# Kernel tuning notes

Measured on AMD Instinct MI355X. Metric: run time of the kernel, lower is better.

## Reference

```python
import jax, jax.numpy as jnp
import numpy as np

S, B, H = 512, 256, 500


def setup_inputs() -> dict:
    key = jax.random.key(0)
    k1, k2, k3, k4, k5 = jax.random.split(key, 5)
    return {
        "hidden": jax.random.normal(k1, (1, B, H), dtype=jnp.float32),
        "encoder_output": jax.random.normal(k2, (S, B, H), dtype=jnp.float32),
        "W_attn": jax.random.normal(k3, (H, 2 * H), dtype=jnp.float32) * 0.02,
        "b_attn": jax.random.normal(k4, (H,), dtype=jnp.float32) * 0.02,
        "v": jax.random.normal(k5, (H,), dtype=jnp.float32),
    }


def reference(hidden, encoder_output, W_attn, b_attn, v):
    # hidden: [1, B, H] -> broadcast to [S, B, H]; concat -> [S, B, 2H]
    s, b, h = encoder_output.shape
    h_exp = jnp.broadcast_to(hidden, (s, b, h))
    cat = jnp.concatenate([h_exp, encoder_output], axis=2)  # [S, B, 2H]
    # Linear(2H -> H) with torch convention W: [out, in], then tanh
    energy = jnp.tanh(jnp.einsum("sbi,hi->sbh", cat, W_attn) + b_attn)  # [S, B, H]
    scores = jnp.einsum("sbh,h->sb", energy, v)  # [S, B]
    attn = jax.nn.softmax(scores.T, axis=1)  # [B, S]
    return attn[:, None, :]  # [B, 1, S]
```

## Files before the change

kernel.cpp:

```cpp
#include <hip/hip_runtime.h>
#include <hip/hip_fp16.h>

#define S_DIM 512
#define B_DIM 256
#define H_DIM 500
#define HP    512
#define M_DIM (S_DIM * B_DIM)

typedef _Float16 half8_t __attribute__((ext_vector_type(8)));
typedef float    f32x4  __attribute__((ext_vector_type(4)));

#define WS_W2I 0
#define WS_AT  (512 * 1024)
#define WS_VP  (1024 * 1024)
#define WS_SC  (1024 * 1024 + 4096)

__device__ __forceinline__ void gld_lds16(const void* g, void* l) {
    __builtin_amdgcn_global_load_lds(
        (const __attribute__((address_space(1))) unsigned int*)g,
        (__attribute__((address_space(3))) unsigned int*)l, 16, 0, 0);
}

__global__ void prep_w2_v(const float* __restrict__ W, const float* __restrict__ v,
                          _Float16* __restrict__ W2img, float* __restrict__ vp) {
    int idx = blockIdx.x * blockDim.x + threadIdx.x;
#pragma unroll
    for (int r = 0; r < 2; ++r) {
        int e = idx + r * 131072;
        int n = e >> 9, k = e & 511;
        float val = (n < H_DIM && k < H_DIM) ? W[n * 1000 + 500 + k] : 0.0f;
        int ks = k >> 5, ce = (k >> 3) & 3, u = k & 7;
        int cL = ce ^ ((n >> 1) & 3);
        W2img[((ks * 512 + n) * 4 + cL) * 8 + u] = (_Float16)val;
    }
    if (idx < HP) vp[idx] = (idx < H_DIM) ? v[idx] : 0.0f;
}

__global__ void prep_A(const float* __restrict__ hidden, const float* __restrict__ W,
                       const float* __restrict__ b_attn, float* __restrict__ At) {
    int b = blockIdx.x;
    int t = threadIdx.x;
    __shared__ float hs[HP];
    hs[t] = (t < H_DIM) ? hidden[b * H_DIM + t] : 0.0f;
    __syncthreads();
    float acc = 0.0f;
    if (t < H_DIM) {
        acc = b_attn[t];
        const float4* wr = (const float4*)(W + t * 1000);
        const float4* hr = (const float4*)hs;
#pragma unroll 5
        for (int i = 0; i < 125; ++i) {
            float4 w4 = wr[i], h4 = hr[i];
            acc += w4.x * h4.x + w4.y * h4.y + w4.z * h4.z + w4.w * h4.w;
        }
    }
    At[t * B_DIM + b] = acc;
}

__launch_bounds__(512, 4)
__global__ void fused_attn_gemm(const float* __restrict__ enc,
                                const _Float16* __restrict__ W2img,
                                const float* __restrict__ At,
                                const float* __restrict__ vp,
                                float* __restrict__ sct) {
    __shared__ _Float16 As[2][64][32];
    __shared__ _Float16 Bs[2][512][32];
    __shared__ float    red[4][64];

    const int tid  = threadIdx.x;
    const int lane = tid & 63;
    const int wid  = tid >> 6;
    const int wm   = wid >> 2;
    const int wn   = wid & 3;
    const int l15  = lane & 15;
    const int lq   = lane >> 4;

    const int mblk  = blockIdx.x;
    const int m0    = mblk * 64;
    const int s_idx = mblk >> 2;
    const int bloc  = (mblk & 3) * 64;

    const bool aw = (tid < 256);
    const int  r  = tid >> 2;
    const int  c  = tid & 3;
    const float* gA = enc + (size_t)(m0 + (r & 63)) * H_DIM + c * 8;
    const int  ca = (c ^ ((r >> 1) & 3)) * 8;

    const int rch = (lq ^ ((l15 >> 1) & 3)) * 8;

    f32x4 a0, a1;
    auto ldA = [&](int kk) {
        if (kk != 480) {
            a0 = *(const f32x4*)(gA + kk);
            a1 = *(const f32x4*)(gA + kk + 4);
        } else {
#pragma unroll
            for (int u = 0; u < 4; ++u) {
                int k = kk + c * 8 + u;
                a0[u] = (k < H_DIM) ? gA[kk + u] : 0.0f;
                a1[u] = (k + 4 < H_DIM) ? gA[kk + 4 + u] : 0.0f;
            }
        }
    };
    auto wrA = [&](int buf) {
        half8_t h;
#pragma unroll
        for (int u = 0; u < 4; ++u) { h[u] = (_Float16)a0[u]; h[u + 4] = (_Float16)a1[u]; }
        *(half8_t*)&As[buf][r & 63][ca] = h;
    };
    auto stB = [&](int buf, int ksrc) {
        const _Float16* gbase = W2img + (size_t)ksrc * 16384;
#pragma unroll
        for (int i = 0; i < 4; ++i) {
            int slotb = wid * 256 + i * 64;
            gld_lds16(gbase + (size_t)(slotb + lane) * 8, (_Float16*)&Bs[buf][0][0] + slotb * 8);
        }
    };

    f32x4 acc[2][8];
#pragma unroll
    for (int a = 0; a < 2; ++a)
#pragma unroll
        for (int b = 0; b < 8; ++b) acc[a][b] = 0;

    stB(0, 0);
    if (aw) { ldA(0); wrA(0); }

    for (int ks = 0; ks < 16; ++ks) {
        const int cur = ks & 1;
        __syncthreads();
        if (ks < 15) {
            stB(cur ^ 1, ks + 1);
            if (aw) ldA((ks + 1) * 32);
        }
        half8_t af0 = *(const half8_t*)&As[cur][wm * 32 + l15][rch];
        half8_t af1 = *(const half8_t*)&As[cur][wm * 32 + 16 + l15][rch];
#pragma unroll
        for (int nf = 0; nf < 8; ++nf) {
            half8_t b = *(const half8_t*)&Bs[cur][wn * 128 + nf * 16 + l15][rch];
            acc[0][nf] = __builtin_amdgcn_mfma_f32_16x16x32_f16(af0, b, acc[0][nf], 0, 0, 0);
            acc[1][nf] = __builtin_amdgcn_mfma_f32_16x16x32_f16(af1, b, acc[1][nf], 0, 0, 0);
        }
        if (ks < 15 && aw) wrA(cur ^ 1);
    }

    float vpv[8];
#pragma unroll
    for (int nf = 0; nf < 8; ++nf) vpv[nf] = vp[wn * 128 + nf * 16 + l15];

    float pj[2][4];
#pragma unroll
    for (int mf = 0; mf < 2; ++mf)
#pragma unroll
        for (int j = 0; j < 4; ++j) pj[mf][j] = 0.0f;

#pragma unroll
    for (int mf = 0; mf < 2; ++mf) {
#pragma unroll
        for (int nf = 0; nf < 8; ++nf) {
            int h = wn * 128 + nf * 16 + l15;
            f32x4 av = *(const f32x4*)(At + h * B_DIM + bloc + wm * 32 + mf * 16 + lq * 4);
#pragma unroll
            for (int j = 0; j < 4; ++j) {
                float x  = acc[mf][nf][j] + av[j];
                float xc = fminf(fmaxf(x, -9.0f), 9.0f);
                float e  = __expf(2.0f * xc);
                float th = (e - 1.0f) / (e + 1.0f);
                pj[mf][j] += vpv[nf] * th;
            }
        }
    }

#pragma unroll
    for (int mf = 0; mf < 2; ++mf)
#pragma unroll
        for (int j = 0; j < 4; ++j) {
            float s = pj[mf][j];
            s += __shfl_xor(s, 1); s += __shfl_xor(s, 2);
            s += __shfl_xor(s, 4); s += __shfl_xor(s, 8);
            if (l15 == 0) red[wn][wm * 32 + mf * 16 + lq * 4 + j] = s;
        }
    __syncthreads();
    if (tid < 64) {
        float p = red[0][tid] + red[1][tid] + red[2][tid] + red[3][tid];
        sct[(size_t)(bloc + tid) * S_DIM + s_idx] = p;
    }
}

__global__ void softmax_rows(const float* __restrict__ sct, float* __restrict__ out) {
    int b = blockIdx.x;
    int t = threadIdx.x;
    int lane = t & 63, w = t >> 6;
    float v = sct[(size_t)b * S_DIM + t];
    float m = v;
#pragma unroll
    for (int off = 1; off < 64; off <<= 1) m = fmaxf(m, __shfl_xor(m, off));
    __shared__ float sm[8], ss[8];
    if (lane == 0) sm[w] = m;
    __syncthreads();
    m = sm[0];
#pragma unroll
    for (int i = 1; i < 8; ++i) m = fmaxf(m, sm[i]);
    float e = __expf(v - m);
    float s = e;
#pragma unroll
    for (int off = 1; off < 64; off <<= 1) s += __shfl_xor(s, off);
    if (lane == 0) ss[w] = s;
    __syncthreads();
    s = ss[0];
#pragma unroll
    for (int i = 1; i < 8; ++i) s += ss[i];
    out[(size_t)b * S_DIM + t] = e / s;
}

extern "C" void kernel_launch(void* const* d_in, const int* in_sizes, int n_in,
                              void* d_out, int out_size, void* d_ws, size_t ws_size,
                              hipStream_t stream) {
    const float* hidden = (const float*)d_in[0];
    const float* enc    = (const float*)d_in[1];
    const float* W      = (const float*)d_in[2];
    const float* b_attn = (const float*)d_in[3];
    const float* v      = (const float*)d_in[4];
    float* out = (float*)d_out;

    char* ws = (char*)d_ws;
    _Float16* W2i = (_Float16*)(ws + WS_W2I);
    float*    At  = (float*)(ws + WS_AT);
    float*    vp  = (float*)(ws + WS_VP);
    float*    sct = (float*)(ws + WS_SC);

    prep_w2_v<<<512, 256, 0, stream>>>(W, v, W2i, vp);
    prep_A<<<256, 512, 0, stream>>>(hidden, W, b_attn, At);
    fused_attn_gemm<<<2048, 512, 0, stream>>>(enc, W2i, At, vp, sct);
    softmax_rows<<<256, 512, 0, stream>>>(sct, out);
}
```

Before: 187.2 us.

## Repartition GEMM warps by N, spread A loads over all threads, hand-pipeline K loop

The fused GEMM now assigns each of the 8 waves a 64-column N slice covering all 64 rows, so B fragments are loaded once per wave and A fragments are shared. The A tile is loaded by all 512 threads with one float4 each, using a register double buffer two slices ahead. The K loop is fully unrolled with explicit vmcnt/lgkmcnt waits and scheduling barriers in place of __syncthreads, so global loads overlap MFMA work. In exchange the code relies on hand-placed waitcnt counts being correct and loads more A fragments per wave.

```diff
diff --git a/kernel.cpp b/kernel.cpp
--- a/kernel.cpp
+++ b/kernel.cpp
@@ -8,6 +8,7 @@
 #define M_DIM (S_DIM * B_DIM)
 
 typedef _Float16 half8_t __attribute__((ext_vector_type(8)));
+typedef _Float16 half4_t __attribute__((ext_vector_type(4)));
 typedef float    f32x4  __attribute__((ext_vector_type(4)));
 
 #define WS_W2I 0
@@ -20,6 +21,10 @@
         (const __attribute__((address_space(1))) unsigned int*)g,
         (__attribute__((address_space(3))) unsigned int*)l, 16, 0, 0);
 }
+
+template<int N> __device__ __forceinline__ void vwait();
+template<> __device__ __forceinline__ void vwait<0>() { asm volatile("s_waitcnt vmcnt(0)" ::: "memory"); }
+template<> __device__ __forceinline__ void vwait<1>() { asm volatile("s_waitcnt vmcnt(1)" ::: "memory"); }
 
 __global__ void prep_w2_v(const float* __restrict__ W, const float* __restrict__ v,
                           _Float16* __restrict__ W2img, float* __restrict__ vp) {
@@ -65,13 +70,11 @@
                                 float* __restrict__ sct) {
     __shared__ _Float16 As[2][64][32];
     __shared__ _Float16 Bs[2][512][32];
-    __shared__ float    red[4][64];
+    __shared__ float    red[8][64];
 
     const int tid  = threadIdx.x;
     const int lane = tid & 63;
     const int wid  = tid >> 6;
-    const int wm   = wid >> 2;
-    const int wn   = wid & 3;
     const int l15  = lane & 15;
     const int lq   = lane >> 4;
 
@@ -80,109 +83,129 @@
     const int s_idx = mblk >> 2;
     const int bloc  = (mblk & 3) * 64;
 
-    const bool aw = (tid < 256);
-    const int  r  = tid >> 2;
-    const int  c  = tid & 3;
-    const float* gA = enc + (size_t)(m0 + (r & 63)) * H_DIM + c * 8;
-    const int  ca = (c ^ ((r >> 1) & 3)) * 8;
+    const int r = tid >> 3;
+    const int j = tid & 7;
+    const float* gA  = enc + (size_t)(m0 + r) * H_DIM + j * 4;
+    const float* gAt = enc + (size_t)(m0 + r) * H_DIM + 480 + (j < 4 ? j : 4) * 4;
+    const bool   jz  = (j >= 5);
+    const int aoff = ((j >> 1) ^ ((r >> 1) & 3)) * 8 + (j & 1) * 4;
 
     const int rch = (lq ^ ((l15 >> 1) & 3)) * 8;
 
-    f32x4 a0, a1;
-    auto ldA = [&](int kk) {
-        if (kk != 480) {
-            a0 = *(const f32x4*)(gA + kk);
-            a1 = *(const f32x4*)(gA + kk + 4);
-        } else {
-#pragma unroll
-            for (int u = 0; u < 4; ++u) {
-                int k = kk + c * 8 + u;
-                a0[u] = (k < H_DIM) ? gA[kk + u] : 0.0f;
-                a1[u] = (k + 4 < H_DIM) ? gA[kk + 4 + u] : 0.0f;
-            }
-        }
-    };
-    auto wrA = [&](int buf) {
-        half8_t h;
-#pragma unroll
-        for (int u = 0; u < 4; ++u) { h[u] = (_Float16)a0[u]; h[u + 4] = (_Float16)a1[u]; }
-        *(half8_t*)&As[buf][r & 63][ca] = h;
+    _Float16* BsLin0 = (_Float16*)&Bs[0][0][0];
+    _Float16* BsLin1 = (_Float16*)&Bs[1][0][0];
+
+    f32x4 acc[4][4];
+#pragma unroll
+    for (int a = 0; a < 4; ++a)
+#pragma unroll
+        for (int b = 0; b < 4; ++b) acc[a][b] = 0;
+
+    auto ldA = [&](int slice) -> f32x4 {
+        return (slice == 15) ? *(const f32x4*)gAt : *(const f32x4*)(gA + slice * 32);
+    };
+    auto wrA = [&](int buf, f32x4 v4, bool tail) {
+        half4_t h;
+#pragma unroll
+        for (int u = 0; u < 4; ++u) h[u] = (tail && jz) ? (_Float16)0.0f : (_Float16)v4[u];
+        *(half4_t*)&As[buf][r][aoff] = h;
     };
     auto stB = [&](int buf, int ksrc) {
         const _Float16* gbase = W2img + (size_t)ksrc * 16384;
+        _Float16* dl = buf ? BsLin1 : BsLin0;
 #pragma unroll
         for (int i = 0; i < 4; ++i) {
             int slotb = wid * 256 + i * 64;
-            gld_lds16(gbase + (size_t)(slotb + lane) * 8, (_Float16*)&Bs[buf][0][0] + slotb * 8);
-        }
-    };
-
-    f32x4 acc[2][8];
-#pragma unroll
-    for (int a = 0; a < 2; ++a)
-#pragma unroll
-        for (int b = 0; b < 8; ++b) acc[a][b] = 0;
-
-    stB(0, 0);
-    if (aw) { ldA(0); wrA(0); }
-
-    for (int ks = 0; ks < 16; ++ks) {
-        const int cur = ks & 1;
-        __syncthreads();
-        if (ks < 15) {
-            stB(cur ^ 1, ks + 1);
-            if (aw) ldA((ks + 1) * 32);
-        }
-        half8_t af0 = *(const half8_t*)&As[cur][wm * 32 + l15][rch];
-        half8_t af1 = *(const half8_t*)&As[cur][wm * 32 + 16 + l15][rch];
-#pragma unroll
-        for (int nf = 0; nf < 8; ++nf) {
-            half8_t b = *(const half8_t*)&Bs[cur][wn * 128 + nf * 16 + l15][rch];
-            acc[0][nf] = __builtin_amdgcn_mfma_f32_16x16x32_f16(af0, b, acc[0][nf], 0, 0, 0);
-            acc[1][nf] = __builtin_amdgcn_mfma_f32_16x16x32_f16(af1, b, acc[1][nf], 0, 0, 0);
-        }
-        if (ks < 15 && aw) wrA(cur ^ 1);
-    }
-
-    float vpv[8];
-#pragma unroll
-    for (int nf = 0; nf < 8; ++nf) vpv[nf] = vp[wn * 128 + nf * 16 + l15];
-
-    float pj[2][4];
-#pragma unroll
-    for (int mf = 0; mf < 2; ++mf)
-#pragma unroll
-        for (int j = 0; j < 4; ++j) pj[mf][j] = 0.0f;
-
-#pragma unroll
-    for (int mf = 0; mf < 2; ++mf) {
-#pragma unroll
-        for (int nf = 0; nf < 8; ++nf) {
-            int h = wn * 128 + nf * 16 + l15;
-            f32x4 av = *(const f32x4*)(At + h * B_DIM + bloc + wm * 32 + mf * 16 + lq * 4);
-#pragma unroll
-            for (int j = 0; j < 4; ++j) {
-                float x  = acc[mf][nf][j] + av[j];
+            gld_lds16(gbase + (size_t)(slotb + lane) * 8, dl + slotb * 8);
+        }
+    };
+    auto compute = [&](int cur) {
+        half8_t af[4];
+#pragma unroll
+        for (int mf = 0; mf < 4; ++mf)
+            af[mf] = *(const half8_t*)&As[cur][mf * 16 + l15][rch];
+#pragma unroll
+        for (int nf = 0; nf < 4; ++nf) {
+            half8_t bq = *(const half8_t*)&Bs[cur][wid * 64 + nf * 16 + l15][rch];
+#pragma unroll
+            for (int mf = 0; mf < 4; ++mf)
+                acc[mf][nf] = __builtin_amdgcn_mfma_f32_16x16x32_f16(af[mf], bq, acc[mf][nf], 0, 0, 0);
+        }
+    };
+
+    f32x4 r0, r1;
+    {
+        f32x4 rA = ldA(0);
+        stB(0, 0);
+        r1 = ldA(1);
+        wrA(0, rA, false);
+    }
+
+#define KSTEP(KS, CUR, RN, RX)                                            \
+    {                                                                     \
+        if ((KS) >= 14) vwait<0>(); else vwait<1>();                      \
+        asm volatile("s_waitcnt lgkmcnt(0)" ::: "memory");                \
+        __builtin_amdgcn_sched_barrier(0);                                \
+        __builtin_amdgcn_s_barrier();                                     \
+        __builtin_amdgcn_sched_barrier(0);                                \
+        if ((KS) + 1 < 16) stB((CUR) ^ 1, (KS) + 1);                      \
+        __builtin_amdgcn_sched_barrier(0);                                \
+        if ((KS) + 2 < 16) RX = ldA((KS) + 2);                            \
+        compute(CUR);                                                     \
+        if ((KS) + 1 < 16) wrA((CUR) ^ 1, RN, (KS) + 1 == 15);            \
+    }
+
+    KSTEP(0, 0, r1, r0)   KSTEP(1, 1, r0, r1)
+    KSTEP(2, 0, r1, r0)   KSTEP(3, 1, r0, r1)
+    KSTEP(4, 0, r1, r0)   KSTEP(5, 1, r0, r1)
+    KSTEP(6, 0, r1, r0)   KSTEP(7, 1, r0, r1)
+    KSTEP(8, 0, r1, r0)   KSTEP(9, 1, r0, r1)
+    KSTEP(10, 0, r1, r0)  KSTEP(11, 1, r0, r1)
+    KSTEP(12, 0, r1, r0)  KSTEP(13, 1, r0, r1)
+    KSTEP(14, 0, r1, r0)  KSTEP(15, 1, r0, r1)
+#undef KSTEP
+
+    float vpv[4];
+#pragma unroll
+    for (int nf = 0; nf < 4; ++nf) vpv[nf] = vp[wid * 64 + nf * 16 + l15];
+
+    float pj[4][4];
+#pragma unroll
+    for (int mf = 0; mf < 4; ++mf)
+#pragma unroll
+        for (int jj = 0; jj < 4; ++jj) pj[mf][jj] = 0.0f;
+
+#pragma unroll
+    for (int mf = 0; mf < 4; ++mf) {
+#pragma unroll
+        for (int nf = 0; nf < 4; ++nf) {
+            int h = wid * 64 + nf * 16 + l15;
+            f32x4 av = *(const f32x4*)(At + h * B_DIM + bloc + mf * 16 + lq * 4);
+#pragma unroll
+            for (int jj = 0; jj < 4; ++jj) {
+                float x  = acc[mf][nf][jj] + av[jj];
                 float xc = fminf(fmaxf(x, -9.0f), 9.0f);
                 float e  = __expf(2.0f * xc);
                 float th = (e - 1.0f) / (e + 1.0f);
-                pj[mf][j] += vpv[nf] * th;
+                pj[mf][jj] += vpv[nf] * th;
             }
         }
     }
 
 #pragma unroll
-    for (int mf = 0; mf < 2; ++mf)
-#pragma unroll
-        for (int j = 0; j < 4; ++j) {
-            float s = pj[mf][j];
+    for (int mf = 0; mf < 4; ++mf)
+#pragma unroll
+        for (int jj = 0; jj < 4; ++jj) {
+            float s = pj[mf][jj];
             s += __shfl_xor(s, 1); s += __shfl_xor(s, 2);
             s += __shfl_xor(s, 4); s += __shfl_xor(s, 8);
-            if (l15 == 0) red[wn][wm * 32 + mf * 16 + lq * 4 + j] = s;
+            if (l15 == 0) red[wid][mf * 16 + lq * 4 + jj] = s;
         }
     __syncthreads();
     if (tid < 64) {
-        float p = red[0][tid] + red[1][tid] + red[2][tid] + red[3][tid];
+        float p = 0.0f;
+#pragma unroll
+        for (int w = 0; w < 8; ++w) p += red[w][tid];
         sct[(size_t)(bloc + tid) * S_DIM + s_idx] = p;
     }
 }
```

New measurement: 213.7 us. 14.1% more time.

## Retile fused attention GEMM to 256x256 blocks with split-N partial scores

Applied to the files above, without the earlier changes.

The fused GEMM+tanh+dot kernel moves from 64-row blocks covering all 512 columns to 256x256 tiles with K=64 steps. Each block writes partial scores for its half of the hidden dimension, and softmax sums the two halves. The B tile now goes through registers instead of direct global-to-LDS loads. The main loop is split into four phases so next-tile loads and LDS writes overlap MFMA work, with raised wave priority and a block-index swizzle for cache locality. The aim is more reuse per LDS byte and better hiding of load latency, at the cost of lower occupancy (2 blocks per CU), 128 KB of LDS and larger register pressure.

```diff
diff --git a/kernel.cpp b/kernel.cpp
--- a/kernel.cpp
+++ b/kernel.cpp
@@ -4,7 +4,6 @@
 #define S_DIM 512
 #define B_DIM 256
 #define H_DIM 500
-#define HP    512
 #define M_DIM (S_DIM * B_DIM)
 
 typedef _Float16 half8_t __attribute__((ext_vector_type(8)));
@@ -15,32 +14,26 @@
 #define WS_VP  (1024 * 1024)
 #define WS_SC  (1024 * 1024 + 4096)
 
-__device__ __forceinline__ void gld_lds16(const void* g, void* l) {
-    __builtin_amdgcn_global_load_lds(
-        (const __attribute__((address_space(1))) unsigned int*)g,
-        (__attribute__((address_space(3))) unsigned int*)l, 16, 0, 0);
-}
-
 __global__ void prep_w2_v(const float* __restrict__ W, const float* __restrict__ v,
-                          _Float16* __restrict__ W2img, float* __restrict__ vp) {
+                          _Float16* __restrict__ W2i, float* __restrict__ vp) {
     int idx = blockIdx.x * blockDim.x + threadIdx.x;
 #pragma unroll
     for (int r = 0; r < 2; ++r) {
         int e = idx + r * 131072;
         int n = e >> 9, k = e & 511;
         float val = (n < H_DIM && k < H_DIM) ? W[n * 1000 + 500 + k] : 0.0f;
-        int ks = k >> 5, ce = (k >> 3) & 3, u = k & 7;
-        int cL = ce ^ ((n >> 1) & 3);
-        W2img[((ks * 512 + n) * 4 + cL) * 8 + u] = (_Float16)val;
-    }
-    if (idx < HP) vp[idx] = (idx < H_DIM) ? v[idx] : 0.0f;
+        int nb = n >> 8, nl = n & 255, kt = k >> 6, c = (k >> 3) & 7, u = k & 7;
+        int cL = c ^ (nl & 7);
+        W2i[(((nb * 8 + kt) * 2048) + nl * 8 + cL) * 8 + u] = (_Float16)val;
+    }
+    if (idx < 512) vp[idx] = (idx < H_DIM) ? v[idx] : 0.0f;
 }
 
 __global__ void prep_A(const float* __restrict__ hidden, const float* __restrict__ W,
                        const float* __restrict__ b_attn, float* __restrict__ At) {
     int b = blockIdx.x;
     int t = threadIdx.x;
-    __shared__ float hs[HP];
+    __shared__ float hs[512];
     hs[t] = (t < H_DIM) ? hidden[b * H_DIM + t] : 0.0f;
     __syncthreads();
     float acc = 0.0f;
@@ -57,15 +50,15 @@
     At[t * B_DIM + b] = acc;
 }
 
-__launch_bounds__(512, 4)
+__launch_bounds__(512, 2)
 __global__ void fused_attn_gemm(const float* __restrict__ enc,
-                                const _Float16* __restrict__ W2img,
+                                const _Float16* __restrict__ W2i,
                                 const float* __restrict__ At,
                                 const float* __restrict__ vp,
                                 float* __restrict__ sct) {
-    __shared__ _Float16 As[2][64][32];
-    __shared__ _Float16 Bs[2][512][32];
-    __shared__ float    red[4][64];
+    __shared__ _Float16 smem_h[65536];
+    _Float16* AsB = smem_h;
+    _Float16* BsB = smem_h + 32768;
 
     const int tid  = threadIdx.x;
     const int lane = tid & 63;
@@ -75,115 +68,166 @@
     const int l15  = lane & 15;
     const int lq   = lane >> 4;
 
-    const int mblk  = blockIdx.x;
-    const int m0    = mblk * 64;
-    const int s_idx = mblk >> 2;
-    const int bloc  = (mblk & 3) * 64;
-
-    const bool aw = (tid < 256);
-    const int  r  = tid >> 2;
-    const int  c  = tid & 3;
-    const float* gA = enc + (size_t)(m0 + (r & 63)) * H_DIM + c * 8;
-    const int  ca = (c ^ ((r >> 1) & 3)) * 8;
-
-    const int rch = (lq ^ ((l15 >> 1) & 3)) * 8;
-
-    f32x4 a0, a1;
-    auto ldA = [&](int kk) {
-        if (kk != 480) {
-            a0 = *(const f32x4*)(gA + kk);
-            a1 = *(const f32x4*)(gA + kk + 4);
+    const int wg   = (blockIdx.x & 7) * 128 + (blockIdx.x >> 3);
+    const int mblk = wg >> 1;
+    const int nblk = wg & 1;
+    const int m0   = mblk * 256;
+
+    const int ra = tid >> 2;
+    const int ja = tid & 3;
+    const size_t rowA0 = (size_t)(m0 + ra) * H_DIM;
+    const size_t rowA1 = (size_t)(m0 + 128 + ra) * H_DIM;
+    const int colb = ja * 16;
+    const int cL0 = ((ja * 2) ^ (ra & 7)) * 8;
+    const int cL1 = ((ja * 2 + 1) ^ (ra & 7)) * 8;
+
+    const _Float16* gWb = W2i + ((size_t)nblk * 8) * 2048 * 8 + (size_t)tid * 8;
+
+    f32x4 acc[8][4];
+#pragma unroll
+    for (int a = 0; a < 8; ++a)
+#pragma unroll
+        for (int b = 0; b < 4; ++b) acc[a][b] = 0;
+
+    f32x4 la0[4], la1[4];
+    half8_t bst[4];
+
+    auto issueB = [&](int kt) {
+        const _Float16* g = gWb + (size_t)kt * 2048 * 8;
+#pragma unroll
+        for (int i = 0; i < 4; ++i) bst[i] = *(const half8_t*)(g + i * 512 * 8);
+    };
+    auto writeB = [&](int buf) {
+#pragma unroll
+        for (int i = 0; i < 4; ++i)
+            *(half8_t*)(BsB + buf * 16384 + (tid + i * 512) * 8) = bst[i];
+    };
+    auto issueA = [&](int kt, int h, f32x4* l) {
+        const float* g = enc + (h ? rowA1 : rowA0);
+        if (kt < 7) {
+            const float* gk = g + kt * 64 + colb;
+#pragma unroll
+            for (int i = 0; i < 4; ++i) l[i] = *(const f32x4*)(gk + i * 4);
         } else {
 #pragma unroll
-            for (int u = 0; u < 4; ++u) {
-                int k = kk + c * 8 + u;
-                a0[u] = (k < H_DIM) ? gA[kk + u] : 0.0f;
-                a1[u] = (k + 4 < H_DIM) ? gA[kk + 4 + u] : 0.0f;
+            for (int i = 0; i < 4; ++i) {
+                int cc = 448 + colb + i * 4;
+                cc = cc > 496 ? 496 : cc;
+                l[i] = *(const f32x4*)(g + cc);
             }
         }
     };
-    auto wrA = [&](int buf) {
-        half8_t h;
-#pragma unroll
-        for (int u = 0; u < 4; ++u) { h[u] = (_Float16)a0[u]; h[u + 4] = (_Float16)a1[u]; }
-        *(half8_t*)&As[buf][r & 63][ca] = h;
-    };
-    auto stB = [&](int buf, int ksrc) {
-        const _Float16* gbase = W2img + (size_t)ksrc * 16384;
-#pragma unroll
-        for (int i = 0; i < 4; ++i) {
-            int slotb = wid * 256 + i * 64;
-            gld_lds16(gbase + (size_t)(slotb + lane) * 8, (_Float16*)&Bs[buf][0][0] + slotb * 8);
-        }
-    };
-
-    f32x4 acc[2][8];
-#pragma unroll
-    for (int a = 0; a < 2; ++a)
-#pragma unroll
-        for (int b = 0; b < 8; ++b) acc[a][b] = 0;
-
-    stB(0, 0);
-    if (aw) { ldA(0); wrA(0); }
-
-    for (int ks = 0; ks < 16; ++ks) {
-        const int cur = ks & 1;
-        __syncthreads();
-        if (ks < 15) {
-            stB(cur ^ 1, ks + 1);
-            if (aw) ldA((ks + 1) * 32);
-        }
-        half8_t af0 = *(const half8_t*)&As[cur][wm * 32 + l15][rch];
-        half8_t af1 = *(const half8_t*)&As[cur][wm * 32 + 16 + l15][rch];
-#pragma unroll
-        for (int nf = 0; nf < 8; ++nf) {
-            half8_t b = *(const half8_t*)&Bs[cur][wn * 128 + nf * 16 + l15][rch];
-            acc[0][nf] = __builtin_amdgcn_mfma_f32_16x16x32_f16(af0, b, acc[0][nf], 0, 0, 0);
-            acc[1][nf] = __builtin_amdgcn_mfma_f32_16x16x32_f16(af1, b, acc[1][nf], 0, 0, 0);
-        }
-        if (ks < 15 && aw) wrA(cur ^ 1);
-    }
-
-    float vpv[8];
-#pragma unroll
-    for (int nf = 0; nf < 8; ++nf) vpv[nf] = vp[wn * 128 + nf * 16 + l15];
-
-    float pj[2][4];
-#pragma unroll
-    for (int mf = 0; mf < 2; ++mf)
-#pragma unroll
-        for (int j = 0; j < 4; ++j) pj[mf][j] = 0.0f;
-
-#pragma unroll
-    for (int mf = 0; mf < 2; ++mf) {
-#pragma unroll
-        for (int nf = 0; nf < 8; ++nf) {
-            int h = wn * 128 + nf * 16 + l15;
-            f32x4 av = *(const f32x4*)(At + h * B_DIM + bloc + wm * 32 + mf * 16 + lq * 4);
+    auto writeA = [&](int buf, int h, const f32x4* l, bool tail) {
+        half8_t h0, h1;
+#pragma unroll
+        for (int u = 0; u < 4; ++u) {
+            h0[u] = (_Float16)l[0][u]; h0[u + 4] = (_Float16)l[1][u];
+            h1[u] = (_Float16)l[2][u]; h1[u + 4] = (_Float16)l[3][u];
+        }
+        if (tail) {
+#pragma unroll
+            for (int u = 0; u < 8; ++u) {
+                if (448 + ja * 16 + u >= H_DIM)     h0[u] = (_Float16)0.0f;
+                if (448 + ja * 16 + 8 + u >= H_DIM) h1[u] = (_Float16)0.0f;
+            }
+        }
+        _Float16* base = AsB + buf * 16384 + (h * 128 + ra) * 64;
+        *(half8_t*)(base + cL0) = h0;
+        *(half8_t*)(base + cL1) = h1;
+    };
+
+#define PHASE(BUF, MH, KS, STAGE)                                              \
+    {                                                                          \
+        half8_t afv[4], bfv[4];                                                \
+        const int rch = (((KS) * 4 + lq) ^ (l15 & 7)) * 8;                     \
+        _Pragma("unroll")                                                      \
+        for (int nf = 0; nf < 4; ++nf)                                         \
+            bfv[nf] = *(const half8_t*)(BsB + (BUF) * 16384 +                  \
+                        (wn * 64 + nf * 16 + l15) * 64 + rch);                 \
+        _Pragma("unroll")                                                      \
+        for (int mf = 0; mf < 4; ++mf)                                         \
+            afv[mf] = *(const half8_t*)(AsB + (BUF) * 16384 +                  \
+                        (wm * 128 + (MH) * 64 + mf * 16 + l15) * 64 + rch);    \
+        STAGE                                                                  \
+        asm volatile("s_barrier" ::: "memory");                                \
+        __builtin_amdgcn_s_setprio(1);                                         \
+        _Pragma("unroll")                                                      \
+        for (int nf = 0; nf < 4; ++nf) {                                       \
+            _Pragma("unroll")                                                  \
+            for (int mf = 0; mf < 4; ++mf)                                     \
+                acc[(MH) * 4 + mf][nf] = __builtin_amdgcn_mfma_f32_16x16x32_f16( \
+                    afv[mf], bfv[nf], acc[(MH) * 4 + mf][nf], 0, 0, 0);        \
+        }                                                                      \
+        __builtin_amdgcn_s_setprio(0);                                         \
+    }
+
+#define TILE(KT, BUF)                                                          \
+    {                                                                          \
+        const bool st = (KT) < 7;                                              \
+        const bool tl = (KT) + 1 == 7;                                         \
+        PHASE(BUF, 0, 0, { if (st) { issueB((KT) + 1); issueA((KT) + 1, 0, la0); } }) \
+        __builtin_amdgcn_s_barrier();                                          \
+        PHASE(BUF, 1, 0, { if (st) { issueA((KT) + 1, 1, la1); } })            \
+        __builtin_amdgcn_s_barrier();                                          \
+        PHASE(BUF, 0, 1, { if (st) { writeB((BUF) ^ 1); writeA((BUF) ^ 1, 0, la0, tl); } }) \
+        __builtin_amdgcn_s_barrier();                                          \
+        PHASE(BUF, 1, 1, { if (st) { writeA((BUF) ^ 1, 1, la1, tl); } })       \
+        asm volatile("s_waitcnt lgkmcnt(0)\n\ts_barrier" ::: "memory");        \
+    }
+
+    issueB(0); issueA(0, 0, la0); issueA(0, 1, la1);
+    writeB(0); writeA(0, 0, la0, false); writeA(0, 1, la1, false);
+    asm volatile("s_waitcnt lgkmcnt(0)\n\ts_barrier" ::: "memory");
+
+    for (int kt = 0; kt < 8; kt += 2) {
+        TILE(kt, 0)
+        TILE(kt + 1, 1)
+    }
+#undef TILE
+#undef PHASE
+
+    const int n0 = nblk * 256;
+    float vpv[4];
+#pragma unroll
+    for (int nf = 0; nf < 4; ++nf) vpv[nf] = vp[n0 + wn * 64 + nf * 16 + l15];
+
+    float pj[8][4];
+#pragma unroll
+    for (int F = 0; F < 8; ++F)
+#pragma unroll
+        for (int j = 0; j < 4; ++j) pj[F][j] = 0.0f;
+
+#pragma unroll
+    for (int F = 0; F < 8; ++F) {
+#pragma unroll
+        for (int nf = 0; nf < 4; ++nf) {
+            int h = n0 + wn * 64 + nf * 16 + l15;
+            f32x4 av = *(const f32x4*)(At + h * B_DIM + wm * 128 + F * 16 + lq * 4);
 #pragma unroll
             for (int j = 0; j < 4; ++j) {
-                float x  = acc[mf][nf][j] + av[j];
+                float x  = acc[F][nf][j] + av[j];
                 float xc = fminf(fmaxf(x, -9.0f), 9.0f);
                 float e  = __expf(2.0f * xc);
                 float th = (e - 1.0f) / (e + 1.0f);
-                pj[mf][j] += vpv[nf] * th;
+                pj[F][j] += vpv[nf] * th;
             }
         }
     }
 
-#pragma unroll
-    for (int mf = 0; mf < 2; ++mf)
+    float* red = (float*)smem_h;
+#pragma unroll
+    for (int F = 0; F < 8; ++F)
 #pragma unroll
         for (int j = 0; j < 4; ++j) {
-            float s = pj[mf][j];
+            float s = pj[F][j];
             s += __shfl_xor(s, 1); s += __shfl_xor(s, 2);
             s += __shfl_xor(s, 4); s += __shfl_xor(s, 8);
-            if (l15 == 0) red[wn][wm * 32 + mf * 16 + lq * 4 + j] = s;
-        }
-    __syncthreads();
-    if (tid < 64) {
-        float p = red[0][tid] + red[1][tid] + red[2][tid] + red[3][tid];
-        sct[(size_t)(bloc + tid) * S_DIM + s_idx] = p;
+            if (l15 == 0) red[wn * 256 + wm * 128 + F * 16 + lq * 4 + j] = s;
+        }
+    __syncthreads();
+    if (tid < 256) {
+        float p = red[tid] + red[256 + tid] + red[512 + tid] + red[768 + tid];
+        sct[(size_t)nblk * M_DIM + (size_t)tid * S_DIM + mblk] = p;
     }
 }
 
@@ -191,7 +235,8 @@
     int b = blockIdx.x;
     int t = threadIdx.x;
     int lane = t & 63, w = t >> 6;
-    float v = sct[(size_t)b * S_DIM + t];
+    size_t idx = (size_t)b * S_DIM + t;
+    float v = sct[idx] + sct[idx + M_DIM];
     float m = v;
 #pragma unroll
     for (int off = 1; off < 64; off <<= 1) m = fmaxf(m, __shfl_xor(m, off));
@@ -231,6 +276,6 @@
 
     prep_w2_v<<<512, 256, 0, stream>>>(W, v, W2i, vp);
     prep_A<<<256, 512, 0, stream>>>(hidden, W, b_attn, At);
-    fused_attn_gemm<<<2048, 512, 0, stream>>>(enc, W2i, At, vp, sct);
+    fused_attn_gemm<<<1024, 512, 0, stream>>>(enc, W2i, At, vp, sct);
     softmax_rows<<<256, 512, 0, stream>>>(sct, out);
 }
```

After: 214.2 us. +14.4%, slower.
